# Kernel optimization log

Hardware: AMD Instinct MI355X
Metric: run time of the kernel (lower is better)

## Reference

```python
import jax, jax.numpy as jnp
import numpy as np

K = 2  # number of propagation hops (SGConv K)


def setup_inputs() -> dict:
    key = jax.random.key(0)
    k1, k2, k3 = jax.random.split(key, 3)
    N, F, C, E = 100000, 64, 40, 1200000
    x = jax.random.normal(k1, (N, F), dtype=jnp.float32)
    edge_index = jax.random.randint(k2, (2, E), 0, N, dtype=jnp.int64)
    W = jax.random.normal(k3, (C, F), dtype=jnp.float32) * (1.0 / np.sqrt(F))
    b = jnp.zeros((C,), dtype=jnp.float32)
    return {"x": x, "edge_index": edge_index, "W": W, "b": b}


def reference(x, edge_index, W, b):
    N = x.shape[0]
    # add self-loops (PyG gcn_norm with add_self_loops=True)
    loop = jnp.arange(N, dtype=edge_index.dtype)
    src = jnp.concatenate([edge_index[0], loop])  # message sources j
    dst = jnp.concatenate([edge_index[1], loop])  # aggregation targets i
    # symmetric normalization: deg over targets, norm_e = d_src^-1/2 * d_dst^-1/2
    deg = jax.ops.segment_sum(jnp.ones_like(src, dtype=x.dtype), dst, num_segments=N)
    dinv = jnp.where(deg > 0, jax.lax.rsqrt(deg), 0.0)
    norm = dinv[src] * dinv[dst]  # [E+N]
    # K-hop propagation: x <- scatter_add(norm * x[src]) at dst
    for _ in range(K):
        x = jax.ops.segment_sum(x[src] * norm[:, None], dst, num_segments=N)
    logits = x @ W.T + b  # [N, C]
    return jax.nn.log_softmax(logits, axis=1)
```

## Files before the change

kernel.cpp:

```cpp
#include <hip/hip_runtime.h>
#include <math.h>

#define FDIM 64
#define CPAD 64
#define NPB  256
#define CAP2B 3456
#define NBMAX 400
#define TILE2 2048
#define EPT2 8
#define PTILE 128


__device__ inline unsigned short f2bf(float f) {
    unsigned int u = __float_as_uint(f);
    unsigned int r = (u + 0x7fffu + ((u >> 16) & 1u)) >> 16;
    return (unsigned short)r;
}
__device__ inline float bf_lo(unsigned int v) { return __uint_as_float(v << 16); }
__device__ inline float bf_hi(unsigned int v) { return __uint_as_float(v & 0xffff0000u); }
__device__ inline unsigned int bfpack(float a, float b) {
    return (unsigned int)f2bf(a) | ((unsigned int)f2bf(b) << 16);
}

__global__ __launch_bounds__(256) void k_zero(int* __restrict__ p, int n) {
    int i = blockIdx.x * 256 + threadIdx.x;
    if (i < n) p[i] = 0;
}


__global__ __launch_bounds__(256) void k_binD(const int* __restrict__ src,
                                              const int* __restrict__ dst,
                                              int* __restrict__ bcnt,
                                              unsigned int* __restrict__ bin2,
                                              int E, int NB) {
    __shared__ int hb[NBMAX];
    __shared__ int hc[NBMAX];
    int tid = threadIdx.x;
    int base = blockIdx.x * TILE2;
    for (int i = tid; i < NB; i += 256) { hb[i] = 0; hc[i] = 0; }
    __syncthreads();
    unsigned int ent[EPT2]; int bk[EPT2];
#pragma unroll
    for (int k = 0; k < EPT2; ++k) {
        int i = base + k * 256 + tid;
        if (i < E) {
            int s = src[i], d = dst[i];
            bk[k] = d >> 8;
            ent[k] = ((unsigned int)s << 8) | (unsigned int)(d & 255);
            atomicAdd(&hb[bk[k]], 1);
        } else bk[k] = -1;
    }
    __syncthreads();
    for (int i = tid; i < NB; i += 256) {
        int c = hb[i];
        hb[i] = (c > 0) ? atomicAdd(&bcnt[i], c) : 0;
    }
    __syncthreads();
#pragma unroll
    for (int k = 0; k < EPT2; ++k) if (bk[k] >= 0) {
        int b = bk[k];
        int pos = hb[b] + atomicAdd(&hc[b], 1);
        if (pos < CAP2B) bin2[(size_t)b * CAP2B + pos] = ent[k];
    }
}


__global__ __launch_bounds__(512) void k_bscan(const int* __restrict__ bcnt,
                                               int* __restrict__ cbase,
                                               int* __restrict__ row_ptr,
                                               int NB, int N, int T) {
    __shared__ int lds[512];
    int tid = threadIdx.x;
    int tot = 0;
    if (tid < NB)
        tot = min(bcnt[tid], CAP2B) + min(NPB, N - tid * NPB);
    lds[tid] = tot;
    __syncthreads();
    int val = tot;
#pragma unroll
    for (int off = 1; off < 512; off <<= 1) {
        int o = (tid >= off) ? lds[tid - off] : 0;
        __syncthreads();
        val += o;
        lds[tid] = val;
        __syncthreads();
    }
    if (tid < NB) cbase[tid] = val - tot;
    if (tid == 0) row_ptr[N] = T;
}

__global__ __launch_bounds__(256) void k_build(const int* __restrict__ bcnt,
                                               const int* __restrict__ cbase,
                                               const unsigned int* __restrict__ bin2,
                                               int* __restrict__ row_ptr,
                                               float* __restrict__ dinv,
                                               int* __restrict__ csr_src, int N) {
    __shared__ int lcnt[256];
    __shared__ int lscan[256];
    __shared__ int lbase[256];
    __shared__ int lcur[256];
    int b = blockIdx.x, tid = threadIdx.x;
    int node = (b << 8) + tid;
    lcnt[tid] = (node < N) ? 1 : 0;
    __syncthreads();
    int M = min(bcnt[b], CAP2B);
    const unsigned int* seg = bin2 + (size_t)b * CAP2B;
    for (int i = tid; i < M; i += 256)
        atomicAdd(&lcnt[seg[i] & 255u], 1);
    __syncthreads();
    int v = lcnt[tid];
    lscan[tid] = v;
    __syncthreads();
    int val = v;
#pragma unroll
    for (int off = 1; off < 256; off <<= 1) {
        int o = (tid >= off) ? lscan[tid - off] : 0;
        __syncthreads();
        val += o;
        lscan[tid] = val;
        __syncthreads();
    }
    int base = cbase[b] + (val - v);
    if (node < N) {
        row_ptr[node] = base;
        dinv[node] = rsqrtf((float)v);
        csr_src[base] = node;
    }
    lbase[tid] = base;
    lcur[tid] = 1;
    __syncthreads();
    for (int i = tid; i < M; i += 256) {
        unsigned int en = seg[i];
        int dl = (int)(en & 255u);
        int pos = lbase[dl] + atomicAdd(&lcur[dl], 1);
        csr_src[pos] = (int)(en >> 8);
    }
}


__global__ __launch_bounds__(256) void k_proj(const float* __restrict__ x,
                                              const float* __restrict__ W,
                                              const float* __restrict__ dinv,
                                              unsigned short* __restrict__ p16,
                                              int N, int C) {
    __shared__ float xs[PTILE][65];
    __shared__ float Wl[40 * 65];
    int tid = threadIdx.x;
    int n0 = blockIdx.x * PTILE;

    for (int i = tid; i < 40 * 64; i += 256) {
        int c = i >> 6, f = i & 63;
        Wl[c * 65 + f] = W[i];
    }
    for (int idx = tid; idx < PTILE * 16; idx += 256) {
        int r = idx >> 4, c4 = (idx & 15) << 2;
        int n = n0 + r;
        float4 v = make_float4(0.f, 0.f, 0.f, 0.f);
        float dn = 0.f;
        if (n < N) {
            v = *(const float4*)&x[(size_t)n * FDIM + c4];
            dn = dinv[n];
        }
        xs[r][c4 + 0] = v.x * dn; xs[r][c4 + 1] = v.y * dn;
        xs[r][c4 + 2] = v.z * dn; xs[r][c4 + 3] = v.w * dn;
    }
    __syncthreads();

    int ng = tid & 31;
    int cg = tid >> 5;
    float acc[4][5];
#pragma unroll
    for (int i = 0; i < 4; ++i)
#pragma unroll
        for (int j = 0; j < 5; ++j) acc[i][j] = 0.f;

#pragma unroll 4
    for (int k = 0; k < FDIM; ++k) {
        float xv[4], wv[5];
#pragma unroll
        for (int i = 0; i < 4; ++i) xv[i] = xs[ng + 32 * i][k];
#pragma unroll
        for (int j = 0; j < 5; ++j) wv[j] = Wl[(cg * 5 + j) * 65 + k];
#pragma unroll
        for (int i = 0; i < 4; ++i)
#pragma unroll
            for (int j = 0; j < 5; ++j)
                acc[i][j] = fmaf(xv[i], wv[j], acc[i][j]);
    }
    __syncthreads();

    unsigned short* ps = (unsigned short*)xs;
#pragma unroll
    for (int i = 0; i < 4; ++i) {
        int r = ng + 32 * i;
#pragma unroll
        for (int j = 0; j < 5; ++j)
            ps[r * 64 + cg * 5 + j] = f2bf(acc[i][j]);
    }
    for (int idx = tid; idx < PTILE * 24; idx += 256) {
        int r = idx / 24, c = 40 + idx % 24;
        ps[r * 64 + c] = 0;
    }
    __syncthreads();
    const unsigned int* pu = (const unsigned int*)ps;
    unsigned int* po = (unsigned int*)p16;
    for (int idx = tid; idx < PTILE * 32; idx += 256) {
        int r = idx >> 5;
        int n = n0 + r;
        if (n < N) po[(size_t)n * 32 + (idx & 31)] = pu[idx];
    }
}


__global__ __launch_bounds__(256) void k_hop1(const int* __restrict__ row_ptr,
                                              const int* __restrict__ csr_src,
                                              const float* __restrict__ dinv,
                                              const uint2* __restrict__ pin2,
                                              uint2* __restrict__ yout2,
                                              int N) {
    int wid = (blockIdx.x << 2) | (threadIdx.x >> 6);
    int lane = threadIdx.x & 63;
    int q = lane >> 4;
    int t = lane & 15;
    if (wid >= N) return;
    int beg = row_ptr[wid], end = row_ptr[wid + 1];

    float a0 = 0.f, a1 = 0.f, a2 = 0.f, a3 = 0.f;
    for (int e0 = beg + q; e0 < end; e0 += 16) {
        int si[4]; uint2 vs[4];
#pragma unroll
        for (int k = 0; k < 4; ++k) {
            int idx = e0 + 4 * k;
            si[k] = (idx < end) ? csr_src[idx] : -1;
        }
#pragma unroll
        for (int k = 0; k < 4; ++k)
            if (si[k] >= 0) vs[k] = pin2[si[k] * 16 + t];
#pragma unroll
        for (int k = 0; k < 4; ++k)
            if (si[k] >= 0) {
                a0 += bf_lo(vs[k].x); a1 += bf_hi(vs[k].x);
                a2 += bf_lo(vs[k].y); a3 += bf_hi(vs[k].y);
            }
    }
    a0 += __shfl_xor(a0, 16); a0 += __shfl_xor(a0, 32);
    a1 += __shfl_xor(a1, 16); a1 += __shfl_xor(a1, 32);
    a2 += __shfl_xor(a2, 16); a2 += __shfl_xor(a2, 32);
    a3 += __shfl_xor(a3, 16); a3 += __shfl_xor(a3, 32);

    if (lane < 16) {
        float dn = dinv[wid];
        float sc = dn * dn;
        yout2[wid * 16 + t] = make_uint2(bfpack(a0 * sc, a1 * sc),
                                         bfpack(a2 * sc, a3 * sc));
    }
}


__global__ __launch_bounds__(256) void k_hop2_lsm(const int* __restrict__ row_ptr,
                                                  const int* __restrict__ csr_src,
                                                  const float* __restrict__ dinv,
                                                  const uint2* __restrict__ pin2,
                                                  const float* __restrict__ b,
                                                  float* __restrict__ out,
                                                  int N, int C) {
    int wid = (blockIdx.x << 2) | (threadIdx.x >> 6);
    int lane = threadIdx.x & 63;
    int q = lane >> 4;
    int t = lane & 15;
    if (wid >= N) return;
    int beg = row_ptr[wid], end = row_ptr[wid + 1];

    float a0 = 0.f, a1 = 0.f, a2 = 0.f, a3 = 0.f;
    for (int e0 = beg + q; e0 < end; e0 += 16) {
        int si[4]; uint2 vs[4];
#pragma unroll
        for (int k = 0; k < 4; ++k) {
            int idx = e0 + 4 * k;
            si[k] = (idx < end) ? csr_src[idx] : -1;
        }
#pragma unroll
        for (int k = 0; k < 4; ++k)
            if (si[k] >= 0) vs[k] = pin2[si[k] * 16 + t];
#pragma unroll
        for (int k = 0; k < 4; ++k)
            if (si[k] >= 0) {
                a0 += bf_lo(vs[k].x); a1 += bf_hi(vs[k].x);
                a2 += bf_lo(vs[k].y); a3 += bf_hi(vs[k].y);
            }
    }
    a0 += __shfl_xor(a0, 16); a0 += __shfl_xor(a0, 32);
    a1 += __shfl_xor(a1, 16); a1 += __shfl_xor(a1, 32);
    a2 += __shfl_xor(a2, 16); a2 += __shfl_xor(a2, 32);
    a3 += __shfl_xor(a3, 16); a3 += __shfl_xor(a3, 32);

    float dn = dinv[wid];
    int c0 = 4 * t;
    bool valid = (c0 < C);
    float l0 = -INFINITY, l1 = -INFINITY, l2 = -INFINITY, l3 = -INFINITY;
    if (valid) {
        l0 = fmaf(a0, dn, b[c0 + 0]);
        l1 = fmaf(a1, dn, b[c0 + 1]);
        l2 = fmaf(a2, dn, b[c0 + 2]);
        l3 = fmaf(a3, dn, b[c0 + 3]);
    }
    float m = fmaxf(fmaxf(l0, l1), fmaxf(l2, l3));
#pragma unroll
    for (int o = 8; o > 0; o >>= 1) m = fmaxf(m, __shfl_xor(m, o));
    float s = valid ? (expf(l0 - m) + expf(l1 - m) + expf(l2 - m) + expf(l3 - m))
                    : 0.0f;
#pragma unroll
    for (int o = 8; o > 0; o >>= 1) s += __shfl_xor(s, o);
    float ls = logf(s);

    if (lane < 16 && valid) {
        float4 r = make_float4(l0 - m - ls, l1 - m - ls, l2 - m - ls, l3 - m - ls);
        *(float4*)&out[(size_t)wid * C + c0] = r;
    }
}


extern "C" void kernel_launch(void* const* d_in, const int* in_sizes, int n_in,
                              void* d_out, int out_size, void* d_ws, size_t ws_size,
                              hipStream_t stream) {
    const float* x  = (const float*)d_in[0];
    const int*   ei = (const int*)d_in[1];
    const float* W  = (const float*)d_in[2];
    const float* b  = (const float*)d_in[3];
    float* out = (float*)d_out;

    const int C = in_sizes[3];
    const int F = in_sizes[2] / C;
    const int N = in_sizes[0] / F;
    const int E = in_sizes[1] / 2;
    (void)F;

    const int* src = ei;
    const int* dst = ei + E;
    const int T  = E + N;
    const int NB = (N + NPB - 1) / NPB;

    char* w8 = (char*)d_ws;
    auto alloc = [&](size_t bytes) {
        char* p = w8;
        w8 += (bytes + 255) & ~(size_t)255;
        return p;
    };
    int*   bcnt    = (int*)  alloc((size_t)NB * 4);
    int*   cbase   = (int*)  alloc((size_t)NB * 4);
    int*   row_ptr = (int*)  alloc((size_t)(N + 1) * 4);
    float* dinv    = (float*)alloc((size_t)N * 4);
    unsigned int* bin2 = (unsigned int*)alloc((size_t)NB * CAP2B * 4);
    int*   csr_src = (int*)  alloc((size_t)T * 4);
    unsigned short* p16 = (unsigned short*)alloc((size_t)N * CPAD * 2);
    uint2* y16     = (uint2*)alloc((size_t)N * 16 * 8);

    const int B = 256;
    const int NT = (E + TILE2 - 1) / TILE2;

    k_zero <<<(NB + B - 1) / B, B, 0, stream>>>(bcnt, NB);
    k_binD <<<NT, B, 0, stream>>>(src, dst, bcnt, bin2, E, NB);
    k_bscan<<<1, 512, 0, stream>>>(bcnt, cbase, row_ptr, NB, N, T);
    k_build<<<NB, B, 0, stream>>>(bcnt, cbase, bin2, row_ptr, dinv, csr_src, N);

    k_proj <<<(N + PTILE - 1) / PTILE, B, 0, stream>>>(x, W, dinv, p16, N, C);

    k_hop1 <<<(N + 3) / 4, B, 0, stream>>>(row_ptr, csr_src, dinv,
                                           (const uint2*)p16, y16, N);

    k_hop2_lsm<<<(N + 3) / 4, B, 0, stream>>>(row_ptr, csr_src, dinv,
                                              (const uint2*)y16, b, out, N, C);
}
```

Measured before the change: 154.7 us.

## Map 8 threads per node with 16-byte gathers in hop kernels

Both propagation kernels now give each destination node an 8-thread group instead of a full 64-lane wavefront. Each thread gathers a 16-byte chunk of the bf16 row, and the group walks the edge list serially 4 at a time. This drops the cross-quarter shuffle reductions and the three quarters of lanes that sat idle during the final write. It also puts 32 nodes in each 256-thread block, and the bias is staged in shared memory. In exchange, each node's edge loop is no longer split across lanes, so per-node latency goes up, and lanes within a wavefront diverge when node degrees differ.

```diff
diff --git a/kernel.cpp b/kernel.cpp
--- a/kernel.cpp
+++ b/kernel.cpp
@@ -215,107 +215,116 @@
 __global__ __launch_bounds__(256) void k_hop1(const int* __restrict__ row_ptr,
                                               const int* __restrict__ csr_src,
                                               const float* __restrict__ dinv,
-                                              const uint2* __restrict__ pin2,
-                                              uint2* __restrict__ yout2,
+                                              const uint4* __restrict__ pin4,
+                                              uint4* __restrict__ yout4,
                                               int N) {
-    int wid = (blockIdx.x << 2) | (threadIdx.x >> 6);
-    int lane = threadIdx.x & 63;
-    int q = lane >> 4;
-    int t = lane & 15;
-    if (wid >= N) return;
-    int beg = row_ptr[wid], end = row_ptr[wid + 1];
+    int g = threadIdx.x >> 3;
+    int t = threadIdx.x & 7;
+    int node = blockIdx.x * 32 + g;
+    if (node >= N) return;
+    int beg = row_ptr[node], end = row_ptr[node + 1];
 
     float a0 = 0.f, a1 = 0.f, a2 = 0.f, a3 = 0.f;
-    for (int e0 = beg + q; e0 < end; e0 += 16) {
-        int si[4]; uint2 vs[4];
+    float a4 = 0.f, a5 = 0.f, a6 = 0.f, a7 = 0.f;
+    for (int e0 = beg; e0 < end; e0 += 4) {
+        int si[4]; uint4 vs[4];
 #pragma unroll
         for (int k = 0; k < 4; ++k) {
-            int idx = e0 + 4 * k;
+            int idx = e0 + k;
             si[k] = (idx < end) ? csr_src[idx] : -1;
         }
 #pragma unroll
         for (int k = 0; k < 4; ++k)
-            if (si[k] >= 0) vs[k] = pin2[si[k] * 16 + t];
+            if (si[k] >= 0) vs[k] = pin4[si[k] * 8 + t];
 #pragma unroll
         for (int k = 0; k < 4; ++k)
             if (si[k] >= 0) {
                 a0 += bf_lo(vs[k].x); a1 += bf_hi(vs[k].x);
                 a2 += bf_lo(vs[k].y); a3 += bf_hi(vs[k].y);
+                a4 += bf_lo(vs[k].z); a5 += bf_hi(vs[k].z);
+                a6 += bf_lo(vs[k].w); a7 += bf_hi(vs[k].w);
             }
     }
-    a0 += __shfl_xor(a0, 16); a0 += __shfl_xor(a0, 32);
-    a1 += __shfl_xor(a1, 16); a1 += __shfl_xor(a1, 32);
-    a2 += __shfl_xor(a2, 16); a2 += __shfl_xor(a2, 32);
-    a3 += __shfl_xor(a3, 16); a3 += __shfl_xor(a3, 32);
-
-    if (lane < 16) {
-        float dn = dinv[wid];
-        float sc = dn * dn;
-        yout2[wid * 16 + t] = make_uint2(bfpack(a0 * sc, a1 * sc),
-                                         bfpack(a2 * sc, a3 * sc));
-    }
+    float dn = dinv[node], sc = dn * dn;
+    yout4[node * 8 + t] = make_uint4(bfpack(a0 * sc, a1 * sc),
+                                     bfpack(a2 * sc, a3 * sc),
+                                     bfpack(a4 * sc, a5 * sc),
+                                     bfpack(a6 * sc, a7 * sc));
 }
 
 
 __global__ __launch_bounds__(256) void k_hop2_lsm(const int* __restrict__ row_ptr,
                                                   const int* __restrict__ csr_src,
                                                   const float* __restrict__ dinv,
-                                                  const uint2* __restrict__ pin2,
-                                                  const float* __restrict__ b,
+                                                  const uint4* __restrict__ pin4,
+                                                  const float* __restrict__ bias,
                                                   float* __restrict__ out,
                                                   int N, int C) {
-    int wid = (blockIdx.x << 2) | (threadIdx.x >> 6);
-    int lane = threadIdx.x & 63;
-    int q = lane >> 4;
-    int t = lane & 15;
-    if (wid >= N) return;
-    int beg = row_ptr[wid], end = row_ptr[wid + 1];
-
-    float a0 = 0.f, a1 = 0.f, a2 = 0.f, a3 = 0.f;
-    for (int e0 = beg + q; e0 < end; e0 += 16) {
-        int si[4]; uint2 vs[4];
+    __shared__ float bl[64];
+    int tid = threadIdx.x;
+    if (tid < 64) bl[tid] = (tid < C) ? bias[tid] : 0.f;
+    __syncthreads();
+
+    int g = tid >> 3;
+    int t = tid & 7;
+    int node = blockIdx.x * 32 + g;
+    if (node >= N) return;
+    int beg = row_ptr[node], end = row_ptr[node + 1];
+
+    float a[8];
+#pragma unroll
+    for (int j = 0; j < 8; ++j) a[j] = 0.f;
+    for (int e0 = beg; e0 < end; e0 += 4) {
+        int si[4]; uint4 vs[4];
 #pragma unroll
         for (int k = 0; k < 4; ++k) {
-            int idx = e0 + 4 * k;
+            int idx = e0 + k;
             si[k] = (idx < end) ? csr_src[idx] : -1;
         }
 #pragma unroll
         for (int k = 0; k < 4; ++k)
-            if (si[k] >= 0) vs[k] = pin2[si[k] * 16 + t];
+            if (si[k] >= 0) vs[k] = pin4[si[k] * 8 + t];
 #pragma unroll
         for (int k = 0; k < 4; ++k)
             if (si[k] >= 0) {
-                a0 += bf_lo(vs[k].x); a1 += bf_hi(vs[k].x);
-                a2 += bf_lo(vs[k].y); a3 += bf_hi(vs[k].y);
+                a[0] += bf_lo(vs[k].x); a[1] += bf_hi(vs[k].x);
+                a[2] += bf_lo(vs[k].y); a[3] += bf_hi(vs[k].y);
+                a[4] += bf_lo(vs[k].z); a[5] += bf_hi(vs[k].z);
+                a[6] += bf_lo(vs[k].w); a[7] += bf_hi(vs[k].w);
             }
     }
-    a0 += __shfl_xor(a0, 16); a0 += __shfl_xor(a0, 32);
-    a1 += __shfl_xor(a1, 16); a1 += __shfl_xor(a1, 32);
-    a2 += __shfl_xor(a2, 16); a2 += __shfl_xor(a2, 32);
-    a3 += __shfl_xor(a3, 16); a3 += __shfl_xor(a3, 32);
-
-    float dn = dinv[wid];
-    int c0 = 4 * t;
+
+    float dn = dinv[node];
+    int c0 = 8 * t;
     bool valid = (c0 < C);
-    float l0 = -INFINITY, l1 = -INFINITY, l2 = -INFINITY, l3 = -INFINITY;
+    float l[8];
+#pragma unroll
+    for (int j = 0; j < 8; ++j)
+        l[j] = valid ? fmaf(a[j], dn, bl[c0 + j]) : -INFINITY;
+
+    float m = l[0];
+#pragma unroll
+    for (int j = 1; j < 8; ++j) m = fmaxf(m, l[j]);
+    m = fmaxf(m, __shfl_xor(m, 1));
+    m = fmaxf(m, __shfl_xor(m, 2));
+    m = fmaxf(m, __shfl_xor(m, 4));
+
+    float s = 0.f;
     if (valid) {
-        l0 = fmaf(a0, dn, b[c0 + 0]);
-        l1 = fmaf(a1, dn, b[c0 + 1]);
-        l2 = fmaf(a2, dn, b[c0 + 2]);
-        l3 = fmaf(a3, dn, b[c0 + 3]);
-    }
-    float m = fmaxf(fmaxf(l0, l1), fmaxf(l2, l3));
-#pragma unroll
-    for (int o = 8; o > 0; o >>= 1) m = fmaxf(m, __shfl_xor(m, o));
-    float s = valid ? (expf(l0 - m) + expf(l1 - m) + expf(l2 - m) + expf(l3 - m))
-                    : 0.0f;
-#pragma unroll
-    for (int o = 8; o > 0; o >>= 1) s += __shfl_xor(s, o);
-    float ls = logf(s);
-
-    if (lane < 16 && valid) {
-        float4 r = make_float4(l0 - m - ls, l1 - m - ls, l2 - m - ls, l3 - m - ls);
-        *(float4*)&out[(size_t)wid * C + c0] = r;
+#pragma unroll
+        for (int j = 0; j < 8; ++j) s += expf(l[j] - m);
+    }
+    s += __shfl_xor(s, 1);
+    s += __shfl_xor(s, 2);
+    s += __shfl_xor(s, 4);
+    float ls = m + logf(s);
+
+    if (valid) {
+        float* op = out + (size_t)node * C + c0;
+        float4 r0 = make_float4(l[0] - ls, l[1] - ls, l[2] - ls, l[3] - ls);
+        float4 r1 = make_float4(l[4] - ls, l[5] - ls, l[6] - ls, l[7] - ls);
+        *(float4*)op = r0;
+        *(float4*)(op + 4) = r1;
     }
 }
 
@@ -353,7 +362,7 @@
     unsigned int* bin2 = (unsigned int*)alloc((size_t)NB * CAP2B * 4);
     int*   csr_src = (int*)  alloc((size_t)T * 4);
     unsigned short* p16 = (unsigned short*)alloc((size_t)N * CPAD * 2);
-    uint2* y16     = (uint2*)alloc((size_t)N * 16 * 8);
+    uint4* y16     = (uint4*)alloc((size_t)N * 8 * 16);
 
     const int B = 256;
     const int NT = (E + TILE2 - 1) / TILE2;
@@ -365,9 +374,9 @@
 
     k_proj <<<(N + PTILE - 1) / PTILE, B, 0, stream>>>(x, W, dinv, p16, N, C);
 
-    k_hop1 <<<(N + 3) / 4, B, 0, stream>>>(row_ptr, csr_src, dinv,
-                                           (const uint2*)p16, y16, N);
-
-    k_hop2_lsm<<<(N + 3) / 4, B, 0, stream>>>(row_ptr, csr_src, dinv,
-                                              (const uint2*)y16, b, out, N, C);
-}
+    k_hop1 <<<(N + 31) / 32, B, 0, stream>>>(row_ptr, csr_src, dinv,
+                                             (const uint4*)p16, y16, N);
+
+    k_hop2_lsm<<<(N + 31) / 32, B, 0, stream>>>(row_ptr, csr_src, dinv,
+                                                (const uint4*)y16, b, out, N, C);
+}
```

Result: faster. 130.1 us (-15.9%).
